# Kernel optimization log

Measured on AMD Instinct MI355X. Metric: run time of the kernel, lower is better.

Reference implementation:

```python
import jax, jax.numpy as jnp
import numpy as np

D_MODEL = 1024
NUM_HEADS = 16
DEPTH = D_MODEL // NUM_HEADS
BATCH = 2
SEQ = 2048


def setup_inputs() -> dict:
    key = jax.random.key(0)
    ks = jax.random.split(key, 12)
    s = 1.0 / np.sqrt(D_MODEL)
    inp = {
        'v': jax.random.normal(ks[0], (BATCH, SEQ, D_MODEL), jnp.float32),
        'k': jax.random.normal(ks[1], (BATCH, SEQ, D_MODEL), jnp.float32),
        'q': jax.random.normal(ks[2], (BATCH, SEQ, D_MODEL), jnp.float32),
        # causal mask: 1.0 where attention is disallowed (strict upper triangle)
        'mask': jnp.triu(jnp.ones((1, 1, SEQ, SEQ), jnp.float32), k=1),
        'Wq': jax.random.normal(ks[3], (D_MODEL, D_MODEL), jnp.float32) * s,
        'bq': jnp.zeros((D_MODEL,), jnp.float32),
        'Wk': jax.random.normal(ks[4], (D_MODEL, D_MODEL), jnp.float32) * s,
        'bk': jnp.zeros((D_MODEL,), jnp.float32),
        'Wv': jax.random.normal(ks[5], (D_MODEL, D_MODEL), jnp.float32) * s,
        'bv': jnp.zeros((D_MODEL,), jnp.float32),
        'Wo': jax.random.normal(ks[6], (D_MODEL, D_MODEL), jnp.float32) * s,
        'bo': jnp.zeros((D_MODEL,), jnp.float32),
    }
    return inp


def _split_heads(x):
    b, s, _ = x.shape
    return x.reshape(b, s, NUM_HEADS, DEPTH).transpose(0, 2, 1, 3)  # [B,H,S,Dh]


def reference(v, k, q, mask, Wq, bq, Wk, bk, Wv, bv, Wo, bo):
    b = q.shape[0]
    qh = _split_heads(q @ Wq.T + bq)
    kh = _split_heads(k @ Wk.T + bk)
    vh = _split_heads(v @ Wv.T + bv)
    scores = jnp.einsum('bhsd,bhtd->bhst', qh, kh) / jnp.sqrt(
        jnp.asarray(DEPTH, jnp.float32))
    scores = scores + mask * (-1e9)
    attn = jax.nn.softmax(scores, axis=-1)
    out = jnp.einsum('bhst,bhtd->bhsd', attn, vh)
    out = out.transpose(0, 2, 1, 3).reshape(b, -1, D_MODEL)
    return out @ Wo.T + bo
```

## Files before the change

kernel.cpp:

```cpp
#include <hip/hip_runtime.h>
#include <hip/hip_bf16.h>

#define D_MODEL 1024
#define NHEADS 16
#define DEPTH 64
#define BATCH 2
#define SEQ 2048
#define NTOK (BATCH * SEQ)

#define QSCALE 0.180336884f
#define DEFER_THR 11.5415603f

typedef short bf16x8 __attribute__((ext_vector_type(8)));
typedef float f32x4 __attribute__((ext_vector_type(4)));
typedef float f32x16 __attribute__((ext_vector_type(16)));
typedef unsigned short ushortx8 __attribute__((ext_vector_type(8)));
typedef unsigned uint2v __attribute__((ext_vector_type(2)));

using gas_ptr = const __attribute__((address_space(1))) unsigned int*;
using las_ptr = __attribute__((address_space(3))) unsigned int*;

__device__ __forceinline__ unsigned short f2bf(float f) {
    union { float f; unsigned u; } v; v.f = f;
    unsigned r = v.u + 0x7fffu + ((v.u >> 16) & 1u);
    return (unsigned short)(r >> 16);
}

__device__ __forceinline__ unsigned cvtpk(float lo, float hi) {
    unsigned r;
    asm("v_cvt_pk_bf16_f32 %0, %1, %2" : "=v"(r) : "v"(lo), "v"(hi));
    return r;
}

__device__ __forceinline__ uint2v pls(unsigned a, unsigned b) {
    return __builtin_amdgcn_permlane32_swap(a, b, false, false);
}

__device__ __forceinline__ void gload16(const void* g, void* l) {
    __builtin_amdgcn_global_load_lds((gas_ptr)g, (las_ptr)l, 16, 0, 0);
}

__global__ __launch_bounds__(256) void convert_bf16(
    const float* __restrict__ q, const float* __restrict__ k, const float* __restrict__ v,
    const float* __restrict__ wq, const float* __restrict__ wk,
    const float* __restrict__ wv, const float* __restrict__ wo,
    unsigned short* __restrict__ qb, unsigned short* __restrict__ kb,
    unsigned short* __restrict__ vb,
    unsigned short* __restrict__ wqb, unsigned short* __restrict__ wkb,
    unsigned short* __restrict__ wvb, unsigned short* __restrict__ wob)
{
    const int ACT = (NTOK * D_MODEL) / 8;
    const int WT  = (D_MODEL * D_MODEL) / 8;
    const int total = 3 * ACT + 4 * WT;
    for (int i = blockIdx.x * 256 + threadIdx.x; i < total; i += gridDim.x * 256) {
        const float* s; unsigned short* d; int off; float sc = 1.f;
        if (i < ACT)            { s = q; d = qb; off = i; }
        else if (i < 2 * ACT)   { s = k; d = kb; off = i - ACT; }
        else if (i < 3 * ACT)   { s = v; d = vb; off = i - 2 * ACT; }
        else {
            int j = i - 3 * ACT;
            int wsel = j >> 17;  off = j & (WT - 1);
            s = (wsel == 0) ? wq : (wsel == 1) ? wk : (wsel == 2) ? wv : wo;
            d = (wsel == 0) ? wqb : (wsel == 1) ? wkb : (wsel == 2) ? wvb : wob;
            if (wsel == 0) sc = QSCALE;
        }
        float4 a = ((const float4*)s)[off * 2];
        float4 b = ((const float4*)s)[off * 2 + 1];
        ushortx8 r;
        r[0] = f2bf(a.x * sc); r[1] = f2bf(a.y * sc);
        r[2] = f2bf(a.z * sc); r[3] = f2bf(a.w * sc);
        r[4] = f2bf(b.x * sc); r[5] = f2bf(b.y * sc);
        r[6] = f2bf(b.z * sc); r[7] = f2bf(b.w * sc);
        ((ushortx8*)d)[off] = r;
    }
}

template<int IT, int DEST, bool QKV>
__global__ __launch_bounds__(256) void gemm_bf16(
    const unsigned short* __restrict__ A0, const unsigned short* __restrict__ A1,
    const unsigned short* __restrict__ A2,
    const unsigned short* __restrict__ B0, const unsigned short* __restrict__ B1,
    const unsigned short* __restrict__ B2,
    const float* __restrict__ bias0, const float* __restrict__ bias1,
    const float* __restrict__ bias2,
    void* __restrict__ C0, void* __restrict__ C1, void* __restrict__ C2,
    int M, int N, int K)
{
    constexpr int BM = IT * 32;
    constexpr int WROWS = IT * 16;
    __shared__ unsigned short As[2][BM * 32];
    __shared__ unsigned short Bs[2][128 * 32];

    const unsigned short* A = A0; const unsigned short* Bw = B0;
    const float* bias = bias0;    void* Cp = C0;
    float bsc = 1.f;
    int zz = 0;
    if (QKV) {
        zz = blockIdx.z;
        if (zz == 0) bsc = QSCALE;
        if (zz == 1) { A = A1; Bw = B1; bias = bias1; Cp = C1; }
        else if (zz == 2) { A = A2; Bw = B2; bias = bias2; Cp = C2; }
    }

    const int tid  = threadIdx.x;
    const int lane = tid & 63;
    const int w    = tid >> 6;
    const int wu   = __builtin_amdgcn_readfirstlane(w);
    const int wr   = w >> 1, wc = w & 1;
    const int lr   = lane & 15, lg = lane >> 4;

    const int row0 = blockIdx.y * BM;
    const int n0   = blockIdx.x * 128;

    const int cA0 = wu * 64 + lane;
    const unsigned short* gA0 = A + (size_t)(row0 + (cA0 >> 2)) * K + (cA0 & 3) * 8;
    const unsigned short* gA1 = nullptr;
    if (IT == 4) {
        const int cA1 = 256 + cA0;
        gA1 = A + (size_t)(row0 + (cA1 >> 2)) * K + (cA1 & 3) * 8;
    }
    const unsigned short* gB0 = Bw + (size_t)(n0 + (cA0 >> 2)) * K + (cA0 & 3) * 8;
    const unsigned short* gB1;
    {
        const int cB1 = 256 + cA0;
        gB1 = Bw + (size_t)(n0 + (cB1 >> 2)) * K + (cB1 & 3) * 8;
    }

    auto STAGE = [&](int kt, int buf) {
        gload16(gA0 + kt, &As[buf][wu * 512]);
        if (IT == 4) gload16(gA1 + kt, &As[buf][2048 + wu * 512]);
        gload16(gB0 + kt, &Bs[buf][wu * 512]);
        gload16(gB1 + kt, &Bs[buf][2048 + wu * 512]);
    };

    f32x4 acc[IT][4];
    for (int i = 0; i < IT; ++i)
        for (int j = 0; j < 4; ++j)
            for (int r = 0; r < 4; ++r) acc[i][j][r] = 0.f;

    STAGE(0, 0);
    __syncthreads();

    const int NT = K / 32;
    int cur = 0;
    for (int t = 0; t < NT; ++t) {
        if (t + 1 < NT) STAGE((t + 1) * 32, cur ^ 1);

        bf16x8 af[IT], bfr[4];
#pragma unroll
        for (int i = 0; i < IT; ++i)
            af[i] = *(const bf16x8*)&As[cur][(wr * WROWS + i * 16 + lr) * 32 + lg * 8];
#pragma unroll
        for (int j = 0; j < 4; ++j)
            bfr[j] = *(const bf16x8*)&Bs[cur][(wc * 64 + j * 16 + lr) * 32 + lg * 8];
#pragma unroll
        for (int i = 0; i < IT; ++i)
#pragma unroll
            for (int j = 0; j < 4; ++j)
                acc[i][j] = __builtin_amdgcn_mfma_f32_16x16x32_bf16(
                    af[i], bfr[j], acc[i][j], 0, 0, 0);

        __syncthreads();
        cur ^= 1;
    }

    for (int i = 0; i < IT; ++i) {
        for (int j = 0; j < 4; ++j) {
            int gcol = n0 + wc * 64 + j * 16 + lr;
            float bv = bias[gcol] * bsc;
            int s0full = row0 + wr * WROWS + i * 16 + lg * 4;
            if (QKV && zz == 1) {
                int b_ = s0full >> 11, sr = s0full & (SEQ - 1);
                int h_ = gcol >> 6, dh = gcol & 63;
                int jt_ = sr >> 6, t0 = sr & 63;
                int tb_ = t0 >> 5, m0 = t0 & 31;
                int dk_ = dh >> 4, hi_ = (dh >> 3) & 1, e_ = dh & 7;
                unsigned short* Kf = (unsigned short*)Cp;
                size_t base = ((size_t)(b_ * NHEADS + h_) * (SEQ >> 6) + jt_) * 4096
                            + (size_t)((tb_ * 4 + dk_) * 64 + hi_ * 32) * 8 + e_;
#pragma unroll
                for (int r = 0; r < 4; ++r)
                    Kf[base + (size_t)(m0 + r) * 8] = f2bf(acc[i][j][r] + bv);
            } else if (QKV && zz == 2) {
                int b_ = s0full >> 11, sr = s0full & (SEQ - 1);
                int h_ = gcol >> 6, dh = gcol & 63;
                int jt_ = sr >> 6, t0 = sr & 63;
                int ts_ = t0 >> 4, hi_ = (t0 >> 3) & 1, e0 = t0 & 7;
                int dblk = dh >> 5, m_ = dh & 31;
                unsigned w0 = (unsigned)f2bf(acc[i][j][0] + bv)
                            | ((unsigned)f2bf(acc[i][j][1] + bv) << 16);
                unsigned w1 = (unsigned)f2bf(acc[i][j][2] + bv)
                            | ((unsigned)f2bf(acc[i][j][3] + bv) << 16);
                unsigned long long pk = (unsigned long long)w0
                                      | ((unsigned long long)w1 << 32);
                unsigned short* Vf = (unsigned short*)Cp;
                size_t idx = ((size_t)(b_ * NHEADS + h_) * (SEQ >> 6) + jt_) * 4096
                           + (size_t)((dblk * 4 + ts_) * 64 + hi_ * 32 + m_) * 8 + e0;
                *(unsigned long long*)&Vf[idx] = pk;
            } else if (DEST == 0) {
#pragma unroll
                for (int r = 0; r < 4; ++r) {
                    int grow = s0full + r;
                    float val = acc[i][j][r] + bv;
                    int b_ = grow >> 11, s = grow & (SEQ - 1);
                    int h_ = gcol >> 6, dh = gcol & 63;
                    ((unsigned short*)Cp)[(((size_t)b_ * NHEADS + h_) * SEQ + s) * DEPTH + dh]
                        = f2bf(val);
                }
            } else {
#pragma unroll
                for (int r = 0; r < 4; ++r) {
                    int grow = s0full + r;
                    ((float*)Cp)[(size_t)grow * N + gcol] = acc[i][j][r] + bv;
                }
            }
        }
    }
}

#define KLOAD(JT, KF)                                                          \
{                                                                              \
    const unsigned short* Kt_ = Kb + (size_t)(JT) * 4096;                      \
    _Pragma("unroll")                                                          \
    for (int f_ = 0; f_ < 8; ++f_)                                             \
        KF[f_] = *(const bf16x8*)&Kt_[(size_t)f_ * 512 + lane * 8];            \
}

#define TILE_BODY(KC, KN)                                                      \
{                                                                              \
    const unsigned short* Vg = Vb + (size_t)jt * 4096;                         \
    bf16x8 vf0[4], vf1[4];                                                     \
    _Pragma("unroll")                                                          \
    for (int ts = 0; ts < 4; ++ts) {                                           \
        vf0[ts] = *(const bf16x8*)&Vg[(size_t)ts * 512 + lane * 8];            \
        vf1[ts] = *(const bf16x8*)&Vg[(size_t)(4 + ts) * 512 + lane * 8];      \
    }                                                                          \
    if (jt + 2 < ntiles) { KLOAD(jt + 2, KN) }                                 \
    f32x16 st[2];                                                              \
    __builtin_amdgcn_s_setprio(1);                                             \
    _Pragma("unroll")                                                          \
    for (int tb = 0; tb < 2; ++tb) {                                           \
        f32x16 a;                                                              \
        _Pragma("unroll") for (int r = 0; r < 16; ++r) a[r] = 0.f;             \
        _Pragma("unroll")                                                      \
        for (int dk = 0; dk < 4; ++dk)                                         \
            a = __builtin_amdgcn_mfma_f32_32x32x16_bf16(KC[tb * 4 + dk], qf[dk], a, 0, 0, 0); \
        st[tb] = a;                                                            \
    }                                                                          \
    __builtin_amdgcn_s_setprio(0);                                             \
    if (jt == ntiles - 1) {                                                    \
        _Pragma("unroll")                                                      \
        for (int tb = 0; tb < 2; ++tb)                                         \
            _Pragma("unroll")                                                  \
            for (int r = 0; r < 16; ++r) {                                     \
                int t = jt * 64 + tb * 32 + (r & 3) + 8 * (r >> 2) + 4 * hi;   \
                if (t > qr0 + m) st[tb][r] = -1e9f;                            \
            }                                                                  \
    }                                                                          \
    float tmx[16];                                                             \
    _Pragma("unroll")                                                          \
    for (int r = 0; r < 16; ++r) tmx[r] = fmaxf(st[0][r], st[1][r]);           \
    _Pragma("unroll")                                                          \
    for (int sft = 8; sft; sft >>= 1)                                          \
        _Pragma("unroll")                                                      \
        for (int r = 0; r < 8; ++r)                                            \
            if (r < sft) tmx[r] = fmaxf(tmx[r], tmx[r + sft]);                 \
    float tmax;                                                                \
    {                                                                          \
        union { float f; unsigned u; } cu_; cu_.f = tmx[0];                    \
        uint2v rr_ = pls(cu_.u, cu_.u);                                        \
        union { unsigned u; float f; } a_, b_; a_.u = rr_[0]; b_.u = rr_[1];   \
        tmax = fmaxf(a_.f, b_.f);                                              \
    }                                                                          \
    if (!__all(tmax <= mrun + DEFER_THR)) {                                    \
        float mnew = fmaxf(mrun, tmax);                                        \
        float sc = exp2f(mrun - mnew);                                         \
        mrun = mnew; lrun *= sc;                                               \
        if (hi == 0) scbw[m] = sc;                                             \
        f32x4 s4[4];                                                           \
        _Pragma("unroll")                                                      \
        for (int g = 0; g < 4; ++g) s4[g] = *(f32x4*)&scbw[g * 8 + hi * 4];    \
        _Pragma("unroll")                                                      \
        for (int r = 0; r < 16; ++r) {                                         \
            float f = s4[r >> 2][r & 3];                                       \
            o0[r] *= f; o1[r] *= f;                                            \
        }                                                                      \
    }                                                                          \
    float psum = 0.f;                                                          \
    _Pragma("unroll")                                                          \
    for (int tb = 0; tb < 2; ++tb)                                             \
        _Pragma("unroll")                                                      \
        for (int r = 0; r < 16; ++r) {                                         \
            float p = exp2f(st[tb][r] - mrun);                                 \
            st[tb][r] = p; psum += p;                                          \
        }                                                                      \
    {                                                                          \
        union { float f; unsigned u; } cu_; cu_.f = psum;                      \
        uint2v rr_ = pls(cu_.u, cu_.u);                                        \
        union { unsigned u; float f; } a_, b_; a_.u = rr_[0]; b_.u = rr_[1];   \
        lrun += a_.f + b_.f;                                                   \
    }                                                                          \
    unsigned pkw[8][2];                                                        \
    _Pragma("unroll")                                                          \
    for (int G = 0; G < 8; ++G) {                                              \
        const int tb = G >> 2, g = G & 3;                                      \
        pkw[G][0] = cvtpk(st[tb][4 * g + 0], st[tb][4 * g + 1]);               \
        pkw[G][1] = cvtpk(st[tb][4 * g + 2], st[tb][4 * g + 3]);               \
    }                                                                          \
    __builtin_amdgcn_s_setprio(1);                                             \
    _Pragma("unroll")                                                          \
    for (int ts = 0; ts < 4; ++ts) {                                           \
        uint2v s0_ = pls(pkw[2 * ts][0], pkw[2 * ts + 1][0]);                  \
        uint2v s1_ = pls(pkw[2 * ts][1], pkw[2 * ts + 1][1]);                  \
        union { unsigned u[4]; bf16x8 v; } uu;                                 \
        uu.u[0] = s0_[0]; uu.u[1] = s1_[0]; uu.u[2] = s0_[1]; uu.u[3] = s1_[1]; \
        o0 = __builtin_amdgcn_mfma_f32_32x32x16_bf16(uu.v, vf0[ts], o0, 0, 0, 0); \
        o1 = __builtin_amdgcn_mfma_f32_32x32x16_bf16(uu.v, vf1[ts], o1, 0, 0, 0); \
    }                                                                          \
    __builtin_amdgcn_s_setprio(0);                                             \
}

__global__ __launch_bounds__(128, 2) void attn_wave(
    const unsigned short* __restrict__ Qh, const unsigned short* __restrict__ Kh,
    const unsigned short* __restrict__ Vt, unsigned short* __restrict__ ctx)
{
    __shared__ __align__(16) float scb[2][32];
    __shared__ __align__(16) float mlbuf[2][2][32];
    __shared__ __align__(16) float c0b[32], c1b[32], invb[32];
    __shared__ __align__(16) float osh0[16][64], osh1[16][64];

    const int tid  = threadIdx.x;
    const int ww   = tid >> 6;
    const int lane = tid & 63;
    const int m    = lane & 31;
    const int hi   = lane >> 5;
    float* scbw = scb[ww];

    const int bid  = blockIdx.x;
    const int bh   = bid & 31;
    const int qb   = 63 - (bid >> 5);
    const int qr0  = qb * 32;

    const int b = bh >> 4, h = bh & 15;
    const unsigned short* Qb = Qh + ((size_t)bh * SEQ + qr0) * DEPTH;
    const unsigned short* Kb = Kh + (size_t)bh * SEQ * DEPTH;
    const unsigned short* Vb = Vt + (size_t)bh * SEQ * DEPTH;

    bf16x8 qf[4];
#pragma unroll
    for (int dk = 0; dk < 4; ++dk)
        qf[dk] = *(const bf16x8*)&Qb[(size_t)m * DEPTH + dk * 16 + hi * 8];

    f32x16 o0, o1;
#pragma unroll
    for (int r = 0; r < 16; ++r) { o0[r] = 0.f; o1[r] = 0.f; }
    float mrun = -1e30f, lrun = 0.f;

    const int ntiles = (qb >> 1) + 1;
    bf16x8 kfA[8], kfB[8];

    int jt = ww;
    if (jt < ntiles) {
        KLOAD(jt, kfA)
        while (true) {
            TILE_BODY(kfA, kfB)
            jt += 2; if (jt >= ntiles) break;
            TILE_BODY(kfB, kfA)
            jt += 2; if (jt >= ntiles) break;
        }
    }

    if (hi == 0) { mlbuf[ww][0][m] = mrun; mlbuf[ww][1][m] = lrun; }
    __syncthreads();
    if (ww == 0 && hi == 0) {
        float m0 = mlbuf[0][0][m], l0 = mlbuf[0][1][m];
        float m1 = mlbuf[1][0][m], l1 = mlbuf[1][1][m];
        float M  = fmaxf(m0, m1);
        float c0 = exp2f(m0 - M), c1 = exp2f(m1 - M);
        c0b[m] = c0; c1b[m] = c1;
        invb[m] = 1.0f / (l0 * c0 + l1 * c1);
    }
    __syncthreads();

    const float* cb = (ww == 0) ? c0b : c1b;
    f32x4 fc[4];
#pragma unroll
    for (int g = 0; g < 4; ++g)
        fc[g] = *(const f32x4*)&cb[g * 8 + hi * 4];
#pragma unroll
    for (int r = 0; r < 16; ++r) {
        float f = fc[r >> 2][r & 3];
        o0[r] *= f; o1[r] *= f;
    }
    if (ww == 0) {
#pragma unroll
        for (int r = 0; r < 16; ++r) { osh0[r][lane] = o0[r]; osh1[r][lane] = o1[r]; }
    }
    __syncthreads();
    if (ww == 1) {
        f32x4 fi[4];
#pragma unroll
        for (int g = 0; g < 4; ++g)
            fi[g] = *(const f32x4*)&invb[g * 8 + hi * 4];
#pragma unroll
        for (int r = 0; r < 16; ++r) {
            float inv = fi[r >> 2][r & 3];
            int ml = (r & 3) + 8 * (r >> 2) + 4 * hi;
            size_t rowbase = ((size_t)b * SEQ + qr0 + ml) * D_MODEL + h * DEPTH;
            ctx[rowbase + m]      = f2bf((o0[r] + osh0[r][lane]) * inv);
            ctx[rowbase + 32 + m] = f2bf((o1[r] + osh1[r][lane]) * inv);
        }
    }
}

extern "C" void kernel_launch(void* const* d_in, const int* in_sizes, int n_in,
                              void* d_out, int out_size, void* d_ws, size_t ws_size,
                              hipStream_t stream) {
    const float* v  = (const float*)d_in[0];
    const float* k  = (const float*)d_in[1];
    const float* q  = (const float*)d_in[2];
    const float* Wq = (const float*)d_in[4];
    const float* bq = (const float*)d_in[5];
    const float* Wk = (const float*)d_in[6];
    const float* bk = (const float*)d_in[7];
    const float* Wv = (const float*)d_in[8];
    const float* bv = (const float*)d_in[9];
    const float* Wo = (const float*)d_in[10];
    const float* bo = (const float*)d_in[11];

    char* ws = (char*)d_ws;
    const size_t MB = 1024 * 1024;
    unsigned short* Qb  = (unsigned short*)(ws + 0);
    unsigned short* Kb  = (unsigned short*)(ws + 8  * MB);
    unsigned short* Vb  = (unsigned short*)(ws + 16 * MB);
    unsigned short* Wqb = (unsigned short*)(ws + 24 * MB);
    unsigned short* Wkb = (unsigned short*)(ws + 26 * MB);
    unsigned short* Wvb = (unsigned short*)(ws + 28 * MB);
    unsigned short* Wob = (unsigned short*)(ws + 30 * MB);
    unsigned short* Qh  = (unsigned short*)(ws + 32 * MB);
    unsigned short* Kh  = (unsigned short*)(ws + 40 * MB);
    unsigned short* Vtt = (unsigned short*)(ws + 48 * MB);
    unsigned short* ctx = Qb;

    convert_bf16<<<2048, 256, 0, stream>>>(q, k, v, Wq, Wk, Wv, Wo,
                                           Qb, Kb, Vb, Wqb, Wkb, Wvb, Wob);

    gemm_bf16<4, 0, true><<<dim3(8, 32, 3), 256, 0, stream>>>(
        Qb, Kb, Vb, Wqb, Wkb, Wvb, bq, bk, bv,
        (void*)Qh, (void*)Kh, (void*)Vtt, NTOK, D_MODEL, D_MODEL);

    attn_wave<<<dim3(2048), 128, 0, stream>>>(Qh, Kh, Vtt, ctx);

    gemm_bf16<2, 1, false><<<dim3(8, 64), 256, 0, stream>>>(
        ctx, nullptr, nullptr, Wob, nullptr, nullptr, bo, nullptr, nullptr,
        d_out, nullptr, nullptr, NTOK, D_MODEL, D_MODEL);
}
```

Baseline: 118.5 us.

## Split attention KV tiles across four waves per block instead of two

```diff
diff --git a/kernel.cpp b/kernel.cpp
--- a/kernel.cpp
+++ b/kernel.cpp
@@ -235,7 +235,7 @@
         vf0[ts] = *(const bf16x8*)&Vg[(size_t)ts * 512 + lane * 8];            \
         vf1[ts] = *(const bf16x8*)&Vg[(size_t)(4 + ts) * 512 + lane * 8];      \
     }                                                                          \
-    if (jt + 2 < ntiles) { KLOAD(jt + 2, KN) }                                 \
+    if (jt + 4 < ntiles) { KLOAD(jt + 4, KN) }                                 \
     f32x16 st[2];                                                              \
     __builtin_amdgcn_s_setprio(1);                                             \
     _Pragma("unroll")                                                          \
@@ -320,14 +320,15 @@
     __builtin_amdgcn_s_setprio(0);                                             \
 }
 
-__global__ __launch_bounds__(128, 2) void attn_wave(
+__global__ __launch_bounds__(256, 2) void attn_wave(
     const unsigned short* __restrict__ Qh, const unsigned short* __restrict__ Kh,
     const unsigned short* __restrict__ Vt, unsigned short* __restrict__ ctx)
 {
-    __shared__ __align__(16) float scb[2][32];
-    __shared__ __align__(16) float mlbuf[2][2][32];
-    __shared__ __align__(16) float c0b[32], c1b[32], invb[32];
-    __shared__ __align__(16) float osh0[16][64], osh1[16][64];
+    __shared__ __align__(16) float scb[4][32];
+    __shared__ __align__(16) float mlbuf[4][2][32];
+    __shared__ __align__(16) float cbuf[4][32], invb[32];
+    __shared__ __align__(16) float oshA0[16][64], oshA1[16][64];
+    __shared__ __align__(16) float oshB0[16][64], oshB1[16][64];
 
     const int tid  = threadIdx.x;
     const int ww   = tid >> 6;
@@ -364,40 +365,56 @@
         KLOAD(jt, kfA)
         while (true) {
             TILE_BODY(kfA, kfB)
-            jt += 2; if (jt >= ntiles) break;
+            jt += 4; if (jt >= ntiles) break;
             TILE_BODY(kfB, kfA)
-            jt += 2; if (jt >= ntiles) break;
+            jt += 4; if (jt >= ntiles) break;
         }
     }
 
     if (hi == 0) { mlbuf[ww][0][m] = mrun; mlbuf[ww][1][m] = lrun; }
     __syncthreads();
     if (ww == 0 && hi == 0) {
-        float m0 = mlbuf[0][0][m], l0 = mlbuf[0][1][m];
-        float m1 = mlbuf[1][0][m], l1 = mlbuf[1][1][m];
-        float M  = fmaxf(m0, m1);
-        float c0 = exp2f(m0 - M), c1 = exp2f(m1 - M);
-        c0b[m] = c0; c1b[m] = c1;
-        invb[m] = 1.0f / (l0 * c0 + l1 * c1);
+        float mm0 = mlbuf[0][0][m], mm1 = mlbuf[1][0][m];
+        float mm2 = mlbuf[2][0][m], mm3 = mlbuf[3][0][m];
+        float ll0 = mlbuf[0][1][m], ll1 = mlbuf[1][1][m];
+        float ll2 = mlbuf[2][1][m], ll3 = mlbuf[3][1][m];
+        float M = fmaxf(fmaxf(mm0, mm1), fmaxf(mm2, mm3));
+        float c0 = exp2f(mm0 - M), c1 = exp2f(mm1 - M);
+        float c2 = exp2f(mm2 - M), c3 = exp2f(mm3 - M);
+        cbuf[0][m] = c0; cbuf[1][m] = c1; cbuf[2][m] = c2; cbuf[3][m] = c3;
+        invb[m] = 1.0f / (ll0 * c0 + ll1 * c1 + ll2 * c2 + ll3 * c3);
     }
     __syncthreads();
 
-    const float* cb = (ww == 0) ? c0b : c1b;
-    f32x4 fc[4];
-#pragma unroll
-    for (int g = 0; g < 4; ++g)
-        fc[g] = *(const f32x4*)&cb[g * 8 + hi * 4];
-#pragma unroll
-    for (int r = 0; r < 16; ++r) {
-        float f = fc[r >> 2][r & 3];
-        o0[r] *= f; o1[r] *= f;
+    {
+        const float* cb = cbuf[ww];
+        f32x4 fc[4];
+#pragma unroll
+        for (int g = 0; g < 4; ++g)
+            fc[g] = *(const f32x4*)&cb[g * 8 + hi * 4];
+#pragma unroll
+        for (int r = 0; r < 16; ++r) {
+            float f = fc[r >> 2][r & 3];
+            o0[r] *= f; o1[r] *= f;
+        }
     }
     if (ww == 0) {
 #pragma unroll
-        for (int r = 0; r < 16; ++r) { osh0[r][lane] = o0[r]; osh1[r][lane] = o1[r]; }
+        for (int r = 0; r < 16; ++r) { oshA0[r][lane] = o0[r]; oshA1[r][lane] = o1[r]; }
+    } else if (ww == 2) {
+#pragma unroll
+        for (int r = 0; r < 16; ++r) { oshB0[r][lane] = o0[r]; oshB1[r][lane] = o1[r]; }
     }
     __syncthreads();
     if (ww == 1) {
+#pragma unroll
+        for (int r = 0; r < 16; ++r) { oshA0[r][lane] += o0[r]; oshA1[r][lane] += o1[r]; }
+    } else if (ww == 3) {
+#pragma unroll
+        for (int r = 0; r < 16; ++r) { oshB0[r][lane] += o0[r]; oshB1[r][lane] += o1[r]; }
+    }
+    __syncthreads();
+    if (ww == 0) {
         f32x4 fi[4];
 #pragma unroll
         for (int g = 0; g < 4; ++g)
@@ -407,8 +424,8 @@
             float inv = fi[r >> 2][r & 3];
             int ml = (r & 3) + 8 * (r >> 2) + 4 * hi;
             size_t rowbase = ((size_t)b * SEQ + qr0 + ml) * D_MODEL + h * DEPTH;
-            ctx[rowbase + m]      = f2bf((o0[r] + osh0[r][lane]) * inv);
-            ctx[rowbase + 32 + m] = f2bf((o1[r] + osh1[r][lane]) * inv);
+            ctx[rowbase + m]      = f2bf((oshA0[r][lane] + oshB0[r][lane]) * inv);
+            ctx[rowbase + 32 + m] = f2bf((oshA1[r][lane] + oshB1[r][lane]) * inv);
         }
     }
 }
@@ -449,7 +466,7 @@
         Qb, Kb, Vb, Wqb, Wkb, Wvb, bq, bk, bv,
         (void*)Qh, (void*)Kh, (void*)Vtt, NTOK, D_MODEL, D_MODEL);
 
-    attn_wave<<<dim3(2048), 128, 0, stream>>>(Qh, Kh, Vtt, ctx);
+    attn_wave<<<dim3(2048), 256, 0, stream>>>(Qh, Kh, Vtt, ctx);
 
     gemm_bf16<2, 1, false><<<dim3(8, 64), 256, 0, stream>>>(
         ctx, nullptr, nullptr, Wob, nullptr, nullptr, bo, nullptr, nullptr,
```

Result: slower. 121.9 us (+2.9%).

## Fuse fp32-to-bf16 activation conversion into QKV projection GEMM

Applied to the files above, without the earlier changes.

```diff
diff --git a/kernel.cpp b/kernel.cpp
--- a/kernel.cpp
+++ b/kernel.cpp
@@ -40,30 +40,19 @@
     __builtin_amdgcn_global_load_lds((gas_ptr)g, (las_ptr)l, 16, 0, 0);
 }
 
-__global__ __launch_bounds__(256) void convert_bf16(
-    const float* __restrict__ q, const float* __restrict__ k, const float* __restrict__ v,
+__global__ __launch_bounds__(256) void convert_w(
     const float* __restrict__ wq, const float* __restrict__ wk,
     const float* __restrict__ wv, const float* __restrict__ wo,
-    unsigned short* __restrict__ qb, unsigned short* __restrict__ kb,
-    unsigned short* __restrict__ vb,
     unsigned short* __restrict__ wqb, unsigned short* __restrict__ wkb,
     unsigned short* __restrict__ wvb, unsigned short* __restrict__ wob)
 {
-    const int ACT = (NTOK * D_MODEL) / 8;
-    const int WT  = (D_MODEL * D_MODEL) / 8;
-    const int total = 3 * ACT + 4 * WT;
+    const int WT = (D_MODEL * D_MODEL) / 8;
+    const int total = 4 * WT;
     for (int i = blockIdx.x * 256 + threadIdx.x; i < total; i += gridDim.x * 256) {
-        const float* s; unsigned short* d; int off; float sc = 1.f;
-        if (i < ACT)            { s = q; d = qb; off = i; }
-        else if (i < 2 * ACT)   { s = k; d = kb; off = i - ACT; }
-        else if (i < 3 * ACT)   { s = v; d = vb; off = i - 2 * ACT; }
-        else {
-            int j = i - 3 * ACT;
-            int wsel = j >> 17;  off = j & (WT - 1);
-            s = (wsel == 0) ? wq : (wsel == 1) ? wk : (wsel == 2) ? wv : wo;
-            d = (wsel == 0) ? wqb : (wsel == 1) ? wkb : (wsel == 2) ? wvb : wob;
-            if (wsel == 0) sc = QSCALE;
-        }
+        int wsel = i >> 17, off = i & (WT - 1);
+        const float* s = (wsel == 0) ? wq : (wsel == 1) ? wk : (wsel == 2) ? wv : wo;
+        unsigned short* d = (wsel == 0) ? wqb : (wsel == 1) ? wkb : (wsel == 2) ? wvb : wob;
+        float sc = (wsel == 0) ? QSCALE : 1.f;
         float4 a = ((const float4*)s)[off * 2];
         float4 b = ((const float4*)s)[off * 2 + 1];
         ushortx8 r;
@@ -75,10 +64,10 @@
     }
 }
 
-template<int IT, int DEST, bool QKV>
+template<int IT, int DEST, bool QKV, bool AF32>
 __global__ __launch_bounds__(256) void gemm_bf16(
-    const unsigned short* __restrict__ A0, const unsigned short* __restrict__ A1,
-    const unsigned short* __restrict__ A2,
+    const void* __restrict__ A0v, const void* __restrict__ A1v,
+    const void* __restrict__ A2v,
     const unsigned short* __restrict__ B0, const unsigned short* __restrict__ B1,
     const unsigned short* __restrict__ B2,
     const float* __restrict__ bias0, const float* __restrict__ bias1,
@@ -91,15 +80,15 @@
     __shared__ unsigned short As[2][BM * 32];
     __shared__ unsigned short Bs[2][128 * 32];
 
-    const unsigned short* A = A0; const unsigned short* Bw = B0;
+    const void* Av = A0v; const unsigned short* Bw = B0;
     const float* bias = bias0;    void* Cp = C0;
     float bsc = 1.f;
     int zz = 0;
     if (QKV) {
         zz = blockIdx.z;
         if (zz == 0) bsc = QSCALE;
-        if (zz == 1) { A = A1; Bw = B1; bias = bias1; Cp = C1; }
-        else if (zz == 2) { A = A2; Bw = B2; bias = bias2; Cp = C2; }
+        if (zz == 1) { Av = A1v; Bw = B1; bias = bias1; Cp = C1; }
+        else if (zz == 2) { Av = A2v; Bw = B2; bias = bias2; Cp = C2; }
     }
 
     const int tid  = threadIdx.x;
@@ -112,25 +101,45 @@
     const int row0 = blockIdx.y * BM;
     const int n0   = blockIdx.x * 128;
 
-    const int cA0 = wu * 64 + lane;
-    const unsigned short* gA0 = A + (size_t)(row0 + (cA0 >> 2)) * K + (cA0 & 3) * 8;
+    const int cB0 = wu * 64 + lane;
+    const unsigned short* gB0 = Bw + (size_t)(n0 + (cB0 >> 2)) * K + (cB0 & 3) * 8;
+    const unsigned short* gB1 = Bw + (size_t)(n0 + 64 + (cB0 >> 2)) * K + (cB0 & 3) * 8;
+
+    const float* Af = (const float*)Av;
+    const unsigned short* Ab = (const unsigned short*)Av;
+    const int arow = tid >> 3, acol = (tid & 7) * 4;
+    float4 ar[4];
+
+    const unsigned short* gA0 = nullptr;
     const unsigned short* gA1 = nullptr;
-    if (IT == 4) {
-        const int cA1 = 256 + cA0;
-        gA1 = A + (size_t)(row0 + (cA1 >> 2)) * K + (cA1 & 3) * 8;
-    }
-    const unsigned short* gB0 = Bw + (size_t)(n0 + (cA0 >> 2)) * K + (cA0 & 3) * 8;
-    const unsigned short* gB1;
-    {
-        const int cB1 = 256 + cA0;
-        gB1 = Bw + (size_t)(n0 + (cB1 >> 2)) * K + (cB1 & 3) * 8;
-    }
-
-    auto STAGE = [&](int kt, int buf) {
+    if (!AF32) {
+        gA0 = Ab + (size_t)(row0 + (cB0 >> 2)) * K + (cB0 & 3) * 8;
+        if (IT == 4)
+            gA1 = Ab + (size_t)(row0 + 64 + (cB0 >> 2)) * K + (cB0 & 3) * 8;
+    }
+
+    auto A_LOAD = [&](int kt) {
+#pragma unroll
+        for (int p = 0; p < 4; ++p)
+            ar[p] = *(const float4*)&Af[(size_t)(row0 + p * 32 + arow) * K + kt + acol];
+    };
+    auto A_WRITE = [&](int buf) {
+#pragma unroll
+        for (int p = 0; p < 4; ++p) {
+            unsigned lo = cvtpk(ar[p].x, ar[p].y);
+            unsigned hh = cvtpk(ar[p].z, ar[p].w);
+            unsigned long long pk = (unsigned long long)lo
+                                  | ((unsigned long long)hh << 32);
+            *(unsigned long long*)&As[buf][(p * 32 + arow) * 32 + acol] = pk;
+        }
+    };
+    auto STAGE_B = [&](int kt, int buf) {
+        gload16(gB0 + kt, &Bs[buf][wu * 512]);
+        gload16(gB1 + kt, &Bs[buf][2048 + wu * 512]);
+    };
+    auto STAGE_A16 = [&](int kt, int buf) {
         gload16(gA0 + kt, &As[buf][wu * 512]);
         if (IT == 4) gload16(gA1 + kt, &As[buf][2048 + wu * 512]);
-        gload16(gB0 + kt, &Bs[buf][wu * 512]);
-        gload16(gB1 + kt, &Bs[buf][2048 + wu * 512]);
     };
 
     f32x4 acc[IT][4];
@@ -138,13 +147,20 @@
         for (int j = 0; j < 4; ++j)
             for (int r = 0; r < 4; ++r) acc[i][j][r] = 0.f;
 
-    STAGE(0, 0);
+    if constexpr (AF32) { A_LOAD(0); A_WRITE(0); }
+    else                { STAGE_A16(0, 0); }
+    STAGE_B(0, 0);
     __syncthreads();
 
     const int NT = K / 32;
     int cur = 0;
     for (int t = 0; t < NT; ++t) {
-        if (t + 1 < NT) STAGE((t + 1) * 32, cur ^ 1);
+        const bool more = (t + 1 < NT);
+        if (more) {
+            if constexpr (AF32) A_LOAD((t + 1) * 32);
+            else                STAGE_A16((t + 1) * 32, cur ^ 1);
+            STAGE_B((t + 1) * 32, cur ^ 1);
+        }
 
         bf16x8 af[IT], bfr[4];
 #pragma unroll
@@ -160,6 +176,7 @@
                 acc[i][j] = __builtin_amdgcn_mfma_f32_16x16x32_bf16(
                     af[i], bfr[j], acc[i][j], 0, 0, 0);
 
+        if (more) { if constexpr (AF32) A_WRITE(cur ^ 1); }
         __syncthreads();
         cur ^= 1;
     }
@@ -430,28 +447,24 @@
 
     char* ws = (char*)d_ws;
     const size_t MB = 1024 * 1024;
-    unsigned short* Qb  = (unsigned short*)(ws + 0);
-    unsigned short* Kb  = (unsigned short*)(ws + 8  * MB);
-    unsigned short* Vb  = (unsigned short*)(ws + 16 * MB);
-    unsigned short* Wqb = (unsigned short*)(ws + 24 * MB);
-    unsigned short* Wkb = (unsigned short*)(ws + 26 * MB);
-    unsigned short* Wvb = (unsigned short*)(ws + 28 * MB);
-    unsigned short* Wob = (unsigned short*)(ws + 30 * MB);
-    unsigned short* Qh  = (unsigned short*)(ws + 32 * MB);
-    unsigned short* Kh  = (unsigned short*)(ws + 40 * MB);
-    unsigned short* Vtt = (unsigned short*)(ws + 48 * MB);
-    unsigned short* ctx = Qb;
-
-    convert_bf16<<<2048, 256, 0, stream>>>(q, k, v, Wq, Wk, Wv, Wo,
-                                           Qb, Kb, Vb, Wqb, Wkb, Wvb, Wob);
-
-    gemm_bf16<4, 0, true><<<dim3(8, 32, 3), 256, 0, stream>>>(
-        Qb, Kb, Vb, Wqb, Wkb, Wvb, bq, bk, bv,
+    unsigned short* ctx = (unsigned short*)(ws + 0);
+    unsigned short* Wqb = (unsigned short*)(ws + 8  * MB);
+    unsigned short* Wkb = (unsigned short*)(ws + 10 * MB);
+    unsigned short* Wvb = (unsigned short*)(ws + 12 * MB);
+    unsigned short* Wob = (unsigned short*)(ws + 14 * MB);
+    unsigned short* Qh  = (unsigned short*)(ws + 16 * MB);
+    unsigned short* Kh  = (unsigned short*)(ws + 24 * MB);
+    unsigned short* Vtt = (unsigned short*)(ws + 32 * MB);
+
+    convert_w<<<1024, 256, 0, stream>>>(Wq, Wk, Wv, Wo, Wqb, Wkb, Wvb, Wob);
+
+    gemm_bf16<4, 0, true, true><<<dim3(8, 32, 3), 256, 0, stream>>>(
+        q, k, v, Wqb, Wkb, Wvb, bq, bk, bv,
         (void*)Qh, (void*)Kh, (void*)Vtt, NTOK, D_MODEL, D_MODEL);
 
     attn_wave<<<dim3(2048), 128, 0, stream>>>(Qh, Kh, Vtt, ctx);
 
-    gemm_bf16<2, 1, false><<<dim3(8, 64), 256, 0, stream>>>(
+    gemm_bf16<2, 1, false, false><<<dim3(8, 64), 256, 0, stream>>>(
         ctx, nullptr, nullptr, Wob, nullptr, nullptr, bo, nullptr, nullptr,
         d_out, nullptr, nullptr, NTOK, D_MODEL, D_MODEL);
 }
```

Measured after the change: 132.5 us. +11.8%, slower.
